# Kernel optimization log

Hardware: AMD Instinct MI355X
Metric: run time of the kernel (lower is better)

The kernel has to match this reference:

```python
import jax, jax.numpy as jnp
import numpy as np

B, S, D, H = 2, 2048, 1024, 16
DEPTH = D // H


def setup_inputs() -> dict:
    key = jax.random.key(0)
    ks = jax.random.split(key, 12)
    inp = {
        "q": jax.random.normal(ks[0], (B, S, D), jnp.float32),
        "k": jax.random.normal(ks[1], (B, S, D), jnp.float32),
        "v": jax.random.normal(ks[2], (B, S - 1, D), jnp.float32),
        # causal mask for the sliced (S-1, S-1) score grid: 1 where masked out
        "mask": jnp.broadcast_to(
            jnp.triu(jnp.ones((S - 1, S - 1), jnp.float32), k=1), (B, S - 1, S - 1)
        ),
        "Wq": jax.random.normal(ks[3], (D, D), jnp.float32) * 0.02,
        "bq": jnp.zeros((D,), jnp.float32),
        "Wk": jax.random.normal(ks[4], (D, D), jnp.float32) * 0.02,
        "bk": jnp.zeros((D,), jnp.float32),
        "Wv": jax.random.normal(ks[5], (D, D), jnp.float32) * 0.02,
        "bv": jnp.zeros((D,), jnp.float32),
        "Wo": jax.random.normal(ks[6], (D, D), jnp.float32) * 0.02,
        "bo": jnp.zeros((D,), jnp.float32),
    }
    return inp


def _split_heads(x):
    # (B, L, D) -> (B, H, L, depth)
    b, l, _ = x.shape
    return x.reshape(b, l, H, DEPTH).transpose(0, 2, 1, 3)


def reference(q, k, v, mask, Wq, bq, Wk, bk, Wv, bv, Wo, bo):
    qq = q @ Wq + bq            # q_layers[0]
    kk = k @ Wk + bk            # k_layers[0]
    vv = v @ Wv + bv            # wv
    qh, kh, vh = _split_heads(qq), _split_heads(kk), _split_heads(vv)
    # scores: (B, H, S, S) then sliced to (B, H, S-1, S-1) as in the source
    scores = jnp.einsum('bhqd,bhkd->bhqk', qh, kh)[:, :, 1:, :-1]
    scale = 1.0 / jnp.sqrt(jnp.asarray(DEPTH, jnp.float32))
    # original casts to fp64 here; JAX default x64-disabled => computed in fp32
    logits = scores * scale + mask[:, None, :, :] * (-1e9)
    att = jax.nn.softmax(logits, axis=-1)   # (B, H, S-1, S-1)
    ctx = jnp.einsum('bhqk,bhkd->bhqd', att, vh)  # v seq len is S-1
    ctx = ctx.transpose(0, 2, 1, 3).reshape(q.shape[0], -1, D)
    out = ctx @ Wo + bo
    return out, att
```

## Files before the change

### kernel.cpp

```cpp
#include <hip/hip_runtime.h>


typedef __attribute__((ext_vector_type(8))) short bf16x8;
typedef __attribute__((ext_vector_type(4))) float f32x4;

#define MFMA_BF16(A, B, C) __builtin_amdgcn_mfma_f32_16x16x32_bf16(A, B, C, 0, 0, 0)

__device__ __forceinline__ short f2bf(float x) {
    unsigned u = __float_as_uint(x);
    u = u + 0x7FFFu + ((u >> 16) & 1u);
    return (short)(u >> 16);
}
__device__ __forceinline__ float bf2f(short s) {
    return __uint_as_float(((unsigned)(unsigned short)s) << 16);
}
__device__ __forceinline__ int imin(int a, int b) { return a < b ? a : b; }

__global__ __launch_bounds__(256) void transpose_split_kernel(
    const float* __restrict__ W, short* __restrict__ Thi, short* __restrict__ Tlo) {
    __shared__ float tile[32][33];
    const int tx = threadIdx.x & 31, ty = threadIdx.x >> 5;
    const int k0 = blockIdx.x * 32, n0 = blockIdx.y * 32;
#pragma unroll
    for (int p = 0; p < 4; ++p)
        tile[ty + p * 8][tx] = W[(size_t)(k0 + ty + p * 8) * 1024 + n0 + tx];
    __syncthreads();
#pragma unroll
    for (int p = 0; p < 4; ++p) {
        int n = n0 + ty + p * 8, k = k0 + tx;
        float x = tile[tx][ty + p * 8];
        short h = f2bf(x);
        Thi[(size_t)n * 1024 + k] = h;
        if (Tlo) Tlo[(size_t)n * 1024 + k] = f2bf(x - bf2f(h));
    }
}

template <int SPLIT, int OUTMODE>
__global__ __launch_bounds__(256) void gemm_kernel(
    const float* __restrict__ A, int M,
    const short* __restrict__ Bthi, const short* __restrict__ Btlo,
    const float* __restrict__ bias,
    float* __restrict__ Cf, short* __restrict__ Chi, short* __restrict__ Clo) {
    __shared__ __align__(16) short Ash[64 * 40];
    __shared__ __align__(16) short Asl[64 * 40];
    __shared__ __align__(16) short Bsh[64 * 40];
    __shared__ __align__(16) short Bsl[64 * 40];

    const int tid = threadIdx.x;
    const int wave = tid >> 6, lane = tid & 63;
    const int quad = lane >> 4, l16 = lane & 15;
    const int m0 = blockIdx.y * 64, n0 = blockIdx.x * 64;

    const int row_s = tid >> 2;
    const int k_s = (tid & 3) * 8;

    f32x4 acc[4];
#pragma unroll
    for (int s = 0; s < 4; ++s) acc[s] = (f32x4){0.f, 0.f, 0.f, 0.f};

    for (int k0 = 0; k0 < 1024; k0 += 32) {
        __syncthreads();
        {
            int arow = imin(m0 + row_s, M - 1);
            const float* ap = A + (size_t)arow * 1024 + k0 + k_s;
            float4 x0 = *(const float4*)ap;
            float4 x1 = *(const float4*)(ap + 4);
            float xs[8] = {x0.x, x0.y, x0.z, x0.w, x1.x, x1.y, x1.z, x1.w};
            bf16x8 hv, lv;
#pragma unroll
            for (int i2 = 0; i2 < 8; ++i2) {
                short h = f2bf(xs[i2]);
                hv[i2] = h;
                if (SPLIT) lv[i2] = f2bf(xs[i2] - bf2f(h));
            }
            *(bf16x8*)&Ash[row_s * 40 + k_s] = hv;
            if (SPLIT) *(bf16x8*)&Asl[row_s * 40 + k_s] = lv;

            const short* bp = Bthi + (size_t)(n0 + row_s) * 1024 + k0 + k_s;
            *(bf16x8*)&Bsh[row_s * 40 + k_s] = *(const bf16x8*)bp;
            if (SPLIT) {
                const short* bp2 = Btlo + (size_t)(n0 + row_s) * 1024 + k0 + k_s;
                *(bf16x8*)&Bsl[row_s * 40 + k_s] = *(const bf16x8*)bp2;
            }
        }
        __syncthreads();

        bf16x8 ah = *(const bf16x8*)&Ash[(wave * 16 + l16) * 40 + quad * 8];
        bf16x8 al;
        if (SPLIT) al = *(const bf16x8*)&Asl[(wave * 16 + l16) * 40 + quad * 8];
#pragma unroll
        for (int s = 0; s < 4; ++s) {
            bf16x8 bh = *(const bf16x8*)&Bsh[(s * 16 + l16) * 40 + quad * 8];
            acc[s] = MFMA_BF16(ah, bh, acc[s]);
            if (SPLIT) {
                bf16x8 bl = *(const bf16x8*)&Bsl[(s * 16 + l16) * 40 + quad * 8];
                acc[s] = MFMA_BF16(ah, bl, acc[s]);
                acc[s] = MFMA_BF16(al, bh, acc[s]);
            }
        }
    }

#pragma unroll
    for (int s = 0; s < 4; ++s) {
        int col = n0 + s * 16 + l16;
        float bv = bias[col];
#pragma unroll
        for (int r = 0; r < 4; ++r) {
            int row = m0 + wave * 16 + quad * 4 + r;
            if (row < M) {
                float c = acc[s][r] + bv;
                size_t off = (size_t)row * 1024 + col;
                if (OUTMODE == 0) {
                    Cf[off] = c;
                } else if (OUTMODE == 1) {
                    Chi[off] = f2bf(c);
                } else {
                    short h = f2bf(c);
                    Chi[off] = h;
                    Clo[off] = f2bf(c - bf2f(h));
                }
            }
        }
    }
}

__global__ __launch_bounds__(256) void attn_kernel(
    const short* __restrict__ QQh, const short* __restrict__ QQl,
    const short* __restrict__ KKh, const short* __restrict__ KKl,
    const short* __restrict__ VV,
    float* __restrict__ att, float* __restrict__ ctx) {
    __shared__ __align__(16) short Ksh[32 * 72];
    __shared__ __align__(16) short Ksl[32 * 72];
    __shared__ __align__(16) short Vts[64 * 40];
    __shared__ __align__(16) short Ps[4][16 * 40];

    const int tid = threadIdx.x;
    const int wave = tid >> 6, lane = tid & 63;
    const int quad = lane >> 4, l16 = lane & 15;
    const int bx = blockIdx.x;
    const int qt = 31 - (bx & 31);
    const int bh = bx >> 5;
    const int h = bh & 15, b = bh >> 4;
    const int i0 = qt * 64;

    const int i_frag = i0 + wave * 16 + l16;
    const int qrow = imin(i_frag + 1, 2047);
    const size_t qoff = ((size_t)(b * 2048 + qrow)) * 1024 + h * 64;
    const bf16x8 qh0 = *(const bf16x8*)&QQh[qoff + 0 + quad * 8];
    const bf16x8 qh1 = *(const bf16x8*)&QQh[qoff + 32 + quad * 8];
    const bf16x8 ql0 = *(const bf16x8*)&QQl[qoff + 0 + quad * 8];
    const bf16x8 ql1 = *(const bf16x8*)&QQl[qoff + 32 + quad * 8];

    const int i_max = imin(i0 + 63, 2046);
    const int jt_max = i_max >> 5;
    const int wave_imax = imin(i0 + wave * 16 + 15, 2046);
    const int my_rowbase = i0 + wave * 16 + quad * 4;

    const int kst_key = tid >> 3;
    const int kst_dd = (tid & 7) * 8;
    const int vst_key = tid & 31, vst_d0 = (tid >> 5) * 8;

    float lsum[4] = {0.f, 0.f, 0.f, 0.f};

    for (int jt = 0; jt <= jt_max; ++jt) {
        __syncthreads();
        {
            int jg = imin(jt * 32 + kst_key, 2047);
            const size_t koff = ((size_t)(b * 2048 + jg)) * 1024 + h * 64 + kst_dd;
            *(bf16x8*)&Ksh[kst_key * 72 + kst_dd] = *(const bf16x8*)&KKh[koff];
            *(bf16x8*)&Ksl[kst_key * 72 + kst_dd] = *(const bf16x8*)&KKl[koff];
        }
        __syncthreads();
        if (jt * 32 <= wave_imax) {
#pragma unroll
            for (int s = 0; s < 2; ++s) {
                f32x4 sc = (f32x4){0.f, 0.f, 0.f, 0.f};
#pragma unroll
                for (int c = 0; c < 2; ++c) {
                    bf16x8 bh = *(const bf16x8*)&Ksh[(s * 16 + l16) * 72 + c * 32 + quad * 8];
                    bf16x8 bl = *(const bf16x8*)&Ksl[(s * 16 + l16) * 72 + c * 32 + quad * 8];
                    bf16x8 ah = (c == 0) ? qh0 : qh1;
                    bf16x8 al = (c == 0) ? ql0 : ql1;
                    sc = MFMA_BF16(ah, bh, sc);
                    sc = MFMA_BF16(ah, bl, sc);
                    sc = MFMA_BF16(al, bh, sc);
                }
                int j = jt * 32 + s * 16 + l16;
#pragma unroll
                for (int r = 0; r < 4; ++r) {
                    int i = my_rowbase + r;
                    if (j <= i && i <= 2046) lsum[r] += __expf(sc[r] * 0.125f);
                }
            }
        }
    }
#pragma unroll
    for (int m = 1; m < 16; m <<= 1) {
#pragma unroll
        for (int r = 0; r < 4; ++r) lsum[r] += __shfl_xor(lsum[r], m, 64);
    }
    float linv[4];
#pragma unroll
    for (int r = 0; r < 4; ++r) linv[r] = 1.0f / lsum[r];

    f32x4 cacc[4];
#pragma unroll
    for (int t = 0; t < 4; ++t) cacc[t] = (f32x4){0.f, 0.f, 0.f, 0.f};

    for (int jt = 0; jt <= jt_max; ++jt) {
        __syncthreads();
        {
            int jg = imin(jt * 32 + kst_key, 2047);
            const size_t koff = ((size_t)(b * 2048 + jg)) * 1024 + h * 64 + kst_dd;
            *(bf16x8*)&Ksh[kst_key * 72 + kst_dd] = *(const bf16x8*)&KKh[koff];
            *(bf16x8*)&Ksl[kst_key * 72 + kst_dd] = *(const bf16x8*)&KKl[koff];
            int vjg = imin(jt * 32 + vst_key, 2046);
            const size_t voff = ((size_t)(b * 2047 + vjg)) * 1024 + h * 64 + vst_d0;
            bf16x8 vv = *(const bf16x8*)&VV[voff];
#pragma unroll
            for (int q2 = 0; q2 < 8; ++q2) Vts[(vst_d0 + q2) * 40 + vst_key] = vv[q2];
        }
        __syncthreads();
        if (jt * 32 <= wave_imax) {
#pragma unroll
            for (int s = 0; s < 2; ++s) {
                f32x4 sc = (f32x4){0.f, 0.f, 0.f, 0.f};
#pragma unroll
                for (int c = 0; c < 2; ++c) {
                    bf16x8 bh = *(const bf16x8*)&Ksh[(s * 16 + l16) * 72 + c * 32 + quad * 8];
                    bf16x8 bl = *(const bf16x8*)&Ksl[(s * 16 + l16) * 72 + c * 32 + quad * 8];
                    bf16x8 ah = (c == 0) ? qh0 : qh1;
                    bf16x8 al = (c == 0) ? ql0 : ql1;
                    sc = MFMA_BF16(ah, bh, sc);
                    sc = MFMA_BF16(ah, bl, sc);
                    sc = MFMA_BF16(al, bh, sc);
                }
                int j = jt * 32 + s * 16 + l16;
#pragma unroll
                for (int r = 0; r < 4; ++r) {
                    int i = my_rowbase + r;
                    bool valid = (j <= i) && (i <= 2046);
                    float p = valid ? __expf(sc[r] * 0.125f) * linv[r] : 0.0f;
                    if (i <= 2046 && j <= 2046)
                        att[(((size_t)(b * 16 + h)) * 2047 + i) * 2047 + j] = p;
                    Ps[wave][(quad * 4 + r) * 40 + s * 16 + l16] = f2bf(p);
                }
            }
            bf16x8 pa = *(const bf16x8*)&Ps[wave][l16 * 40 + quad * 8];
#pragma unroll
            for (int t = 0; t < 4; ++t) {
                bf16x8 vb = *(const bf16x8*)&Vts[(t * 16 + l16) * 40 + quad * 8];
                cacc[t] = MFMA_BF16(pa, vb, cacc[t]);
            }
        } else {
#pragma unroll
            for (int s = 0; s < 2; ++s) {
                int j = jt * 32 + s * 16 + l16;
#pragma unroll
                for (int r = 0; r < 4; ++r) {
                    int i = my_rowbase + r;
                    if (i <= 2046 && j <= 2046)
                        att[(((size_t)(b * 16 + h)) * 2047 + i) * 2047 + j] = 0.0f;
                }
            }
        }
    }

#pragma unroll
    for (int t = 0; t < 4; ++t) {
#pragma unroll
        for (int r = 0; r < 4; ++r) {
            int i = my_rowbase + r;
            if (i <= 2046)
                ctx[((size_t)(b * 2047 + i)) * 1024 + h * 64 + t * 16 + l16] = cacc[t][r];
        }
    }

    const int js = (jt_max + 1) * 32;
    for (int rr = 0; rr < 64; ++rr) {
        int i = i0 + rr;
        if (i > 2046) break;
        float* rowp = att + (((size_t)(b * 16 + h)) * 2047 + i) * 2047;
        for (int cc = js + tid; cc < 2047; cc += 256) rowp[cc] = 0.0f;
    }
}

extern "C" void kernel_launch(void* const* d_in, const int* in_sizes, int n_in,
                              void* d_out, int out_size, void* d_ws, size_t ws_size,
                              hipStream_t stream) {
    (void)in_sizes; (void)n_in; (void)out_size; (void)ws_size;
    const float* q  = (const float*)d_in[0];
    const float* k  = (const float*)d_in[1];
    const float* v  = (const float*)d_in[2];
    const float* Wq = (const float*)d_in[4];
    const float* bq = (const float*)d_in[5];
    const float* Wk = (const float*)d_in[6];
    const float* bk = (const float*)d_in[7];
    const float* Wv = (const float*)d_in[8];
    const float* bv = (const float*)d_in[9];
    const float* Wo = (const float*)d_in[10];
    const float* bo = (const float*)d_in[11];

    float* out = (float*)d_out;
    float* att = out + (size_t)2 * 2047 * 1024;

    char* ws = (char*)d_ws;
    size_t off = 0;
    auto alloc = [&](size_t bytes) -> void* {
        void* p = ws + off;
        off += (bytes + 255) & ~(size_t)255;
        return p;
    };
    short* Wqt_h = (short*)alloc((size_t)1024 * 1024 * 2);
    short* Wqt_l = (short*)alloc((size_t)1024 * 1024 * 2);
    short* Wkt_h = (short*)alloc((size_t)1024 * 1024 * 2);
    short* Wkt_l = (short*)alloc((size_t)1024 * 1024 * 2);
    short* Wvt_h = (short*)alloc((size_t)1024 * 1024 * 2);
    short* Wot_h = (short*)alloc((size_t)1024 * 1024 * 2);
    short* QQh = (short*)alloc((size_t)4096 * 1024 * 2);
    short* QQl = (short*)alloc((size_t)4096 * 1024 * 2);
    short* KKh = (short*)alloc((size_t)4096 * 1024 * 2);
    short* KKl = (short*)alloc((size_t)4096 * 1024 * 2);
    short* VVp = (short*)alloc((size_t)4094 * 1024 * 2);
    float* CTX = (float*)alloc((size_t)4094 * 1024 * 4);

    dim3 tgrid(32, 32);
    transpose_split_kernel<<<tgrid, 256, 0, stream>>>(Wq, Wqt_h, Wqt_l);
    transpose_split_kernel<<<tgrid, 256, 0, stream>>>(Wk, Wkt_h, Wkt_l);
    transpose_split_kernel<<<tgrid, 256, 0, stream>>>(Wv, Wvt_h, nullptr);
    transpose_split_kernel<<<tgrid, 256, 0, stream>>>(Wo, Wot_h, nullptr);

    dim3 ggrid(16, 64);
    gemm_kernel<1, 2><<<ggrid, 256, 0, stream>>>(q, 4096, Wqt_h, Wqt_l, bq, nullptr, QQh, QQl);
    gemm_kernel<1, 2><<<ggrid, 256, 0, stream>>>(k, 4096, Wkt_h, Wkt_l, bk, nullptr, KKh, KKl);
    gemm_kernel<0, 1><<<ggrid, 256, 0, stream>>>(v, 4094, Wvt_h, nullptr, bv, nullptr, VVp, nullptr);

    attn_kernel<<<dim3(2 * 16 * 32), 256, 0, stream>>>(QQh, QQl, KKh, KKl, VVp, att, CTX);

    gemm_kernel<0, 0><<<ggrid, 256, 0, stream>>>(CTX, 4094, Wot_h, nullptr, bo, out, nullptr, nullptr);
}
```

Before: 1.049 ms.

## Rewrite pipeline with bf16 pre-split inputs, LDS DMA loads, larger tiles, transposed V

Inputs are split to bf16 hi/lo ahead of time so the GEMMs load pre-converted operands straight into LDS with global_load_lds DMA, using 128x64 tiles per block. The attention kernel moves to 64-key tiles and folds the 1/8 scale into the Q projection. Its first pass uses a 2-MFMA approximation for the row sums, V is pre-transposed so its tiles can also be DMA-loaded, and the context is written as bf16. These changes target conversion overhead, the LDS store cost and register shuffles, at the price of extra kernels and workspace. The cheaper row sums and bf16 context also reduce precision.

```diff
diff --git a/kernel.cpp b/kernel.cpp
--- a/kernel.cpp
+++ b/kernel.cpp
@@ -15,6 +15,12 @@
     return __uint_as_float(((unsigned)(unsigned short)s) << 16);
 }
 __device__ __forceinline__ int imin(int a, int b) { return a < b ? a : b; }
+
+__device__ __forceinline__ void dma16(const short* g, short* l) {
+    __builtin_amdgcn_global_load_lds(
+        (const __attribute__((address_space(1))) unsigned int*)g,
+        (__attribute__((address_space(3))) unsigned int*)l, 16, 0, 0);
+}
 
 __global__ __launch_bounds__(256) void transpose_split_kernel(
     const float* __restrict__ W, short* __restrict__ Thi, short* __restrict__ Tlo) {
@@ -35,115 +41,175 @@
     }
 }
 
+__global__ __launch_bounds__(256) void split_kernel(
+    const float* __restrict__ X, short* __restrict__ Hi, short* __restrict__ Lo, int n8) {
+    int idx = blockIdx.x * 256 + threadIdx.x;
+    if (idx >= n8) return;
+    float4 x0 = *((const float4*)X + (size_t)idx * 2);
+    float4 x1 = *((const float4*)X + (size_t)idx * 2 + 1);
+    float xs[8] = {x0.x, x0.y, x0.z, x0.w, x1.x, x1.y, x1.z, x1.w};
+    bf16x8 hv, lv;
+#pragma unroll
+    for (int e = 0; e < 8; ++e) {
+        short h = f2bf(xs[e]);
+        hv[e] = h;
+        lv[e] = f2bf(xs[e] - bf2f(h));
+    }
+    *(bf16x8*)&Hi[(size_t)idx * 8] = hv;
+    if (Lo) *(bf16x8*)&Lo[(size_t)idx * 8] = lv;
+}
+
 template <int SPLIT, int OUTMODE>
-__global__ __launch_bounds__(256) void gemm_kernel(
-    const float* __restrict__ A, int M,
-    const short* __restrict__ Bthi, const short* __restrict__ Btlo,
-    const float* __restrict__ bias,
+__global__ __launch_bounds__(256) void gemm_dma(
+    const short* __restrict__ Ahg, const short* __restrict__ Alg, int M,
+    const short* __restrict__ Bhg, const short* __restrict__ Blg,
+    const float* __restrict__ bias, float scale,
     float* __restrict__ Cf, short* __restrict__ Chi, short* __restrict__ Clo) {
-    __shared__ __align__(16) short Ash[64 * 40];
-    __shared__ __align__(16) short Asl[64 * 40];
-    __shared__ __align__(16) short Bsh[64 * 40];
-    __shared__ __align__(16) short Bsl[64 * 40];
+    __shared__ __align__(16) short Ah[512 * 8];
+    __shared__ __align__(16) short Al[SPLIT ? 512 * 8 : 8];
+    __shared__ __align__(16) short Bh[256 * 8];
+    __shared__ __align__(16) short Bl[SPLIT ? 256 * 8 : 8];
 
     const int tid = threadIdx.x;
-    const int wave = tid >> 6, lane = tid & 63;
+    const int w = tid >> 6, lane = tid & 63;
     const int quad = lane >> 4, l16 = lane & 15;
-    const int m0 = blockIdx.y * 64, n0 = blockIdx.x * 64;
-
-    const int row_s = tid >> 2;
-    const int k_s = (tid & 3) * 8;
-
-    f32x4 acc[4];
-#pragma unroll
-    for (int s = 0; s < 4; ++s) acc[s] = (f32x4){0.f, 0.f, 0.f, 0.f};
+    const int m0 = blockIdx.y * 128, n0 = blockIdx.x * 64;
+    const int row0 = (w & 1) * 64, col0 = (w >> 1) * 32;
+
+    f32x4 acc[4][2];
+#pragma unroll
+    for (int mi = 0; mi < 4; ++mi)
+#pragma unroll
+        for (int ni = 0; ni < 2; ++ni) acc[mi][ni] = (f32x4){0.f, 0.f, 0.f, 0.f};
+
+    const int a_row = tid & 127;
+    const int a_gr = imin(m0 + a_row, M - 1);
+    const int b_gr = n0 + (tid & 63);
+    const int b_c = tid >> 6;
 
     for (int k0 = 0; k0 < 1024; k0 += 32) {
         __syncthreads();
+#pragma unroll
+        for (int p = 0; p < 2; ++p) {
+            int c = (p * 256 + tid) >> 7;
+            const size_t go = (size_t)a_gr * 1024 + k0 + c * 8;
+            dma16(Ahg + go, &Ah[(p * 256 + tid) * 8]);
+            if (SPLIT) dma16(Alg + go, &Al[(p * 256 + tid) * 8]);
+        }
         {
-            int arow = imin(m0 + row_s, M - 1);
-            const float* ap = A + (size_t)arow * 1024 + k0 + k_s;
-            float4 x0 = *(const float4*)ap;
-            float4 x1 = *(const float4*)(ap + 4);
-            float xs[8] = {x0.x, x0.y, x0.z, x0.w, x1.x, x1.y, x1.z, x1.w};
-            bf16x8 hv, lv;
-#pragma unroll
-            for (int i2 = 0; i2 < 8; ++i2) {
-                short h = f2bf(xs[i2]);
-                hv[i2] = h;
-                if (SPLIT) lv[i2] = f2bf(xs[i2] - bf2f(h));
-            }
-            *(bf16x8*)&Ash[row_s * 40 + k_s] = hv;
-            if (SPLIT) *(bf16x8*)&Asl[row_s * 40 + k_s] = lv;
-
-            const short* bp = Bthi + (size_t)(n0 + row_s) * 1024 + k0 + k_s;
-            *(bf16x8*)&Bsh[row_s * 40 + k_s] = *(const bf16x8*)bp;
-            if (SPLIT) {
-                const short* bp2 = Btlo + (size_t)(n0 + row_s) * 1024 + k0 + k_s;
-                *(bf16x8*)&Bsl[row_s * 40 + k_s] = *(const bf16x8*)bp2;
-            }
-        }
-        __syncthreads();
-
-        bf16x8 ah = *(const bf16x8*)&Ash[(wave * 16 + l16) * 40 + quad * 8];
-        bf16x8 al;
-        if (SPLIT) al = *(const bf16x8*)&Asl[(wave * 16 + l16) * 40 + quad * 8];
-#pragma unroll
-        for (int s = 0; s < 4; ++s) {
-            bf16x8 bh = *(const bf16x8*)&Bsh[(s * 16 + l16) * 40 + quad * 8];
-            acc[s] = MFMA_BF16(ah, bh, acc[s]);
-            if (SPLIT) {
-                bf16x8 bl = *(const bf16x8*)&Bsl[(s * 16 + l16) * 40 + quad * 8];
-                acc[s] = MFMA_BF16(ah, bl, acc[s]);
-                acc[s] = MFMA_BF16(al, bh, acc[s]);
-            }
-        }
-    }
-
-#pragma unroll
-    for (int s = 0; s < 4; ++s) {
-        int col = n0 + s * 16 + l16;
+            const size_t go = (size_t)b_gr * 1024 + k0 + b_c * 8;
+            dma16(Bhg + go, &Bh[tid * 8]);
+            if (SPLIT) dma16(Blg + go, &Bl[tid * 8]);
+        }
+        __syncthreads();
+
+        bf16x8 af[4], afl[4], bfr[2], bfl[2];
+#pragma unroll
+        for (int mi = 0; mi < 4; ++mi) {
+            int r = row0 + mi * 16 + l16;
+            af[mi] = *(const bf16x8*)&Ah[(quad * 128 + r) * 8];
+            if (SPLIT) afl[mi] = *(const bf16x8*)&Al[(quad * 128 + r) * 8];
+        }
+#pragma unroll
+        for (int ni = 0; ni < 2; ++ni) {
+            int cdx = col0 + ni * 16 + l16;
+            bfr[ni] = *(const bf16x8*)&Bh[(quad * 64 + cdx) * 8];
+            if (SPLIT) bfl[ni] = *(const bf16x8*)&Bl[(quad * 64 + cdx) * 8];
+        }
+#pragma unroll
+        for (int mi = 0; mi < 4; ++mi)
+#pragma unroll
+            for (int ni = 0; ni < 2; ++ni) {
+                acc[mi][ni] = MFMA_BF16(af[mi], bfr[ni], acc[mi][ni]);
+                if (SPLIT) {
+                    acc[mi][ni] = MFMA_BF16(af[mi], bfl[ni], acc[mi][ni]);
+                    acc[mi][ni] = MFMA_BF16(afl[mi], bfr[ni], acc[mi][ni]);
+                }
+            }
+    }
+
+#pragma unroll
+    for (int ni = 0; ni < 2; ++ni) {
+        int col = n0 + col0 + ni * 16 + l16;
         float bv = bias[col];
 #pragma unroll
-        for (int r = 0; r < 4; ++r) {
-            int row = m0 + wave * 16 + quad * 4 + r;
-            if (row < M) {
-                float c = acc[s][r] + bv;
-                size_t off = (size_t)row * 1024 + col;
-                if (OUTMODE == 0) {
-                    Cf[off] = c;
-                } else if (OUTMODE == 1) {
-                    Chi[off] = f2bf(c);
-                } else {
-                    short h = f2bf(c);
-                    Chi[off] = h;
-                    Clo[off] = f2bf(c - bf2f(h));
-                }
-            }
-        }
+        for (int mi = 0; mi < 4; ++mi) {
+#pragma unroll
+            for (int r = 0; r < 4; ++r) {
+                int row = m0 + row0 + mi * 16 + quad * 4 + r;
+                if (row < M) {
+                    float c = (acc[mi][ni][r] + bv) * scale;
+                    size_t off = (size_t)row * 1024 + col;
+                    if (OUTMODE == 0) {
+                        Cf[off] = c;
+                    } else if (OUTMODE == 1) {
+                        Chi[off] = f2bf(c);
+                    } else {
+                        short h = f2bf(c);
+                        Chi[off] = h;
+                        Clo[off] = f2bf(c - bf2f(h));
+                    }
+                }
+            }
+        }
+    }
+}
+
+__global__ __launch_bounds__(256) void transpose_v_kernel(
+    const short* __restrict__ VV, short* __restrict__ VT) {
+    __shared__ short t[64][72];
+    const int tid = threadIdx.x;
+    const int st = blockIdx.x & 31, bh = blockIdx.x >> 5;
+    const int b = bh >> 4, h = bh & 15;
+    const int s0 = st * 64;
+    {
+        int seq = s0 + (tid >> 2), d0 = (tid & 3) * 16;
+        int seqc = imin(seq, 2046);
+        const short* src = VV + ((size_t)(b * 2047 + seqc)) * 1024 + h * 64 + d0;
+        bf16x8 v0 = *(const bf16x8*)src;
+        bf16x8 v1 = *(const bf16x8*)(src + 8);
+        bool ok = (seq <= 2046);
+#pragma unroll
+        for (int e = 0; e < 8; ++e) {
+            t[d0 + e][tid >> 2] = ok ? v0[e] : (short)0;
+            t[d0 + 8 + e][tid >> 2] = ok ? v1[e] : (short)0;
+        }
+    }
+    __syncthreads();
+    {
+        int d = tid >> 2, sc2 = (tid & 3) * 16;
+        bf16x8 o0, o1;
+#pragma unroll
+        for (int e = 0; e < 8; ++e) {
+            o0[e] = t[d][sc2 + e];
+            o1[e] = t[d][sc2 + 8 + e];
+        }
+        short* dst = VT + ((size_t)(bh * 64 + d)) * 2048 + s0 + sc2;
+        *(bf16x8*)dst = o0;
+        *(bf16x8*)(dst + 8) = o1;
     }
 }
 
 __global__ __launch_bounds__(256) void attn_kernel(
     const short* __restrict__ QQh, const short* __restrict__ QQl,
     const short* __restrict__ KKh, const short* __restrict__ KKl,
-    const short* __restrict__ VV,
-    float* __restrict__ att, float* __restrict__ ctx) {
-    __shared__ __align__(16) short Ksh[32 * 72];
-    __shared__ __align__(16) short Ksl[32 * 72];
-    __shared__ __align__(16) short Vts[64 * 40];
-    __shared__ __align__(16) short Ps[4][16 * 40];
+    const short* __restrict__ VT,
+    float* __restrict__ att, short* __restrict__ CTX) {
+    __shared__ __align__(16) short Kh[512 * 8];
+    __shared__ __align__(16) short Kl[512 * 8];
+    __shared__ __align__(16) short Vt[512 * 8];
+    __shared__ __align__(16) short Ps[4][16 * 72];
 
     const int tid = threadIdx.x;
-    const int wave = tid >> 6, lane = tid & 63;
+    const int w = tid >> 6, lane = tid & 63;
     const int quad = lane >> 4, l16 = lane & 15;
     const int bx = blockIdx.x;
-    const int qt = 31 - (bx & 31);
-    const int bh = bx >> 5;
+    const int qt = 31 - (bx >> 5);
+    const int bh = bx & 31;
     const int h = bh & 15, b = bh >> 4;
     const int i0 = qt * 64;
 
-    const int i_frag = i0 + wave * 16 + l16;
+    const int i_frag = i0 + w * 16 + l16;
     const int qrow = imin(i_frag + 1, 2047);
     const size_t qoff = ((size_t)(b * 2048 + qrow)) * 1024 + h * 64;
     const bf16x8 qh0 = *(const bf16x8*)&QQh[qoff + 0 + quad * 8];
@@ -152,44 +218,40 @@
     const bf16x8 ql1 = *(const bf16x8*)&QQl[qoff + 32 + quad * 8];
 
     const int i_max = imin(i0 + 63, 2046);
-    const int jt_max = i_max >> 5;
-    const int wave_imax = imin(i0 + wave * 16 + 15, 2046);
-    const int my_rowbase = i0 + wave * 16 + quad * 4;
-
-    const int kst_key = tid >> 3;
-    const int kst_dd = (tid & 7) * 8;
-    const int vst_key = tid & 31, vst_d0 = (tid >> 5) * 8;
+    const int jt_max = i_max >> 6;
+    const int wave_imax = imin(i0 + w * 16 + 15, 2046);
+    const int rowbase = i0 + w * 16 + quad * 4;
+
+    const int dma_key = tid & 63;
+    const int dma_cc0 = tid >> 6;
 
     float lsum[4] = {0.f, 0.f, 0.f, 0.f};
 
     for (int jt = 0; jt <= jt_max; ++jt) {
-        __syncthreads();
-        {
-            int jg = imin(jt * 32 + kst_key, 2047);
-            const size_t koff = ((size_t)(b * 2048 + jg)) * 1024 + h * 64 + kst_dd;
-            *(bf16x8*)&Ksh[kst_key * 72 + kst_dd] = *(const bf16x8*)&KKh[koff];
-            *(bf16x8*)&Ksl[kst_key * 72 + kst_dd] = *(const bf16x8*)&KKl[koff];
-        }
-        __syncthreads();
-        if (jt * 32 <= wave_imax) {
-#pragma unroll
-            for (int s = 0; s < 2; ++s) {
+        const int j0 = jt * 64;
+        __syncthreads();
+#pragma unroll
+        for (int p = 0; p < 2; ++p) {
+            int cc = p * 4 + dma_cc0;
+            dma16(KKh + ((size_t)(b * 2048 + j0 + dma_key)) * 1024 + h * 64 + cc * 8,
+                  &Kh[(p * 256 + tid) * 8]);
+        }
+        __syncthreads();
+        if (j0 <= wave_imax) {
+#pragma unroll
+            for (int s = 0; s < 4; ++s) {
                 f32x4 sc = (f32x4){0.f, 0.f, 0.f, 0.f};
 #pragma unroll
                 for (int c = 0; c < 2; ++c) {
-                    bf16x8 bh = *(const bf16x8*)&Ksh[(s * 16 + l16) * 72 + c * 32 + quad * 8];
-                    bf16x8 bl = *(const bf16x8*)&Ksl[(s * 16 + l16) * 72 + c * 32 + quad * 8];
-                    bf16x8 ah = (c == 0) ? qh0 : qh1;
-                    bf16x8 al = (c == 0) ? ql0 : ql1;
-                    sc = MFMA_BF16(ah, bh, sc);
-                    sc = MFMA_BF16(ah, bl, sc);
-                    sc = MFMA_BF16(al, bh, sc);
-                }
-                int j = jt * 32 + s * 16 + l16;
+                    bf16x8 kh = *(const bf16x8*)&Kh[((c * 4 + quad) * 64 + s * 16 + l16) * 8];
+                    sc = MFMA_BF16(c ? qh1 : qh0, kh, sc);
+                    sc = MFMA_BF16(c ? ql1 : ql0, kh, sc);
+                }
+                int j = j0 + s * 16 + l16;
 #pragma unroll
                 for (int r = 0; r < 4; ++r) {
-                    int i = my_rowbase + r;
-                    if (j <= i && i <= 2046) lsum[r] += __expf(sc[r] * 0.125f);
+                    int i = rowbase + r;
+                    if (j <= i && i <= 2046) lsum[r] += __expf(sc[r]);
                 }
             }
         }
@@ -208,59 +270,62 @@
     for (int t = 0; t < 4; ++t) cacc[t] = (f32x4){0.f, 0.f, 0.f, 0.f};
 
     for (int jt = 0; jt <= jt_max; ++jt) {
-        __syncthreads();
-        {
-            int jg = imin(jt * 32 + kst_key, 2047);
-            const size_t koff = ((size_t)(b * 2048 + jg)) * 1024 + h * 64 + kst_dd;
-            *(bf16x8*)&Ksh[kst_key * 72 + kst_dd] = *(const bf16x8*)&KKh[koff];
-            *(bf16x8*)&Ksl[kst_key * 72 + kst_dd] = *(const bf16x8*)&KKl[koff];
-            int vjg = imin(jt * 32 + vst_key, 2046);
-            const size_t voff = ((size_t)(b * 2047 + vjg)) * 1024 + h * 64 + vst_d0;
-            bf16x8 vv = *(const bf16x8*)&VV[voff];
-#pragma unroll
-            for (int q2 = 0; q2 < 8; ++q2) Vts[(vst_d0 + q2) * 40 + vst_key] = vv[q2];
-        }
-        __syncthreads();
-        if (jt * 32 <= wave_imax) {
-#pragma unroll
-            for (int s = 0; s < 2; ++s) {
+        const int j0 = jt * 64;
+        __syncthreads();
+#pragma unroll
+        for (int p = 0; p < 2; ++p) {
+            int cc = p * 4 + dma_cc0;
+            const size_t ko = ((size_t)(b * 2048 + j0 + dma_key)) * 1024 + h * 64 + cc * 8;
+            dma16(KKh + ko, &Kh[(p * 256 + tid) * 8]);
+            dma16(KKl + ko, &Kl[(p * 256 + tid) * 8]);
+            dma16(VT + ((size_t)(bh * 64 + dma_key)) * 2048 + j0 + cc * 8,
+                  &Vt[(p * 256 + tid) * 8]);
+        }
+        __syncthreads();
+        if (j0 <= wave_imax) {
+#pragma unroll
+            for (int s = 0; s < 4; ++s) {
                 f32x4 sc = (f32x4){0.f, 0.f, 0.f, 0.f};
 #pragma unroll
                 for (int c = 0; c < 2; ++c) {
-                    bf16x8 bh = *(const bf16x8*)&Ksh[(s * 16 + l16) * 72 + c * 32 + quad * 8];
-                    bf16x8 bl = *(const bf16x8*)&Ksl[(s * 16 + l16) * 72 + c * 32 + quad * 8];
-                    bf16x8 ah = (c == 0) ? qh0 : qh1;
-                    bf16x8 al = (c == 0) ? ql0 : ql1;
-                    sc = MFMA_BF16(ah, bh, sc);
-                    sc = MFMA_BF16(ah, bl, sc);
-                    sc = MFMA_BF16(al, bh, sc);
-                }
-                int j = jt * 32 + s * 16 + l16;
+                    const int ci = ((c * 4 + quad) * 64 + s * 16 + l16) * 8;
+                    bf16x8 kh = *(const bf16x8*)&Kh[ci];
+                    bf16x8 kl = *(const bf16x8*)&Kl[ci];
+                    bf16x8 ah = c ? qh1 : qh0;
+                    bf16x8 al = c ? ql1 : ql0;
+                    sc = MFMA_BF16(ah, kh, sc);
+                    sc = MFMA_BF16(ah, kl, sc);
+                    sc = MFMA_BF16(al, kh, sc);
+                }
+                int j = j0 + s * 16 + l16;
 #pragma unroll
                 for (int r = 0; r < 4; ++r) {
-                    int i = my_rowbase + r;
+                    int i = rowbase + r;
                     bool valid = (j <= i) && (i <= 2046);
-                    float p = valid ? __expf(sc[r] * 0.125f) * linv[r] : 0.0f;
+                    float p = valid ? __expf(sc[r]) * linv[r] : 0.0f;
                     if (i <= 2046 && j <= 2046)
-                        att[(((size_t)(b * 16 + h)) * 2047 + i) * 2047 + j] = p;
-                    Ps[wave][(quad * 4 + r) * 40 + s * 16 + l16] = f2bf(p);
-                }
-            }
-            bf16x8 pa = *(const bf16x8*)&Ps[wave][l16 * 40 + quad * 8];
-#pragma unroll
-            for (int t = 0; t < 4; ++t) {
-                bf16x8 vb = *(const bf16x8*)&Vts[(t * 16 + l16) * 40 + quad * 8];
-                cacc[t] = MFMA_BF16(pa, vb, cacc[t]);
+                        att[((size_t)bh * 2047 + i) * 2047 + j] = p;
+                    Ps[w][(quad * 4 + r) * 72 + s * 16 + l16] = f2bf(p);
+                }
+            }
+#pragma unroll
+            for (int c = 0; c < 2; ++c) {
+                bf16x8 pa = *(const bf16x8*)&Ps[w][l16 * 72 + c * 32 + quad * 8];
+#pragma unroll
+                for (int t = 0; t < 4; ++t) {
+                    bf16x8 vb = *(const bf16x8*)&Vt[((c * 4 + quad) * 64 + t * 16 + l16) * 8];
+                    cacc[t] = MFMA_BF16(pa, vb, cacc[t]);
+                }
             }
         } else {
 #pragma unroll
-            for (int s = 0; s < 2; ++s) {
-                int j = jt * 32 + s * 16 + l16;
+            for (int s = 0; s < 4; ++s) {
+                int j = j0 + s * 16 + l16;
 #pragma unroll
                 for (int r = 0; r < 4; ++r) {
-                    int i = my_rowbase + r;
+                    int i = rowbase + r;
                     if (i <= 2046 && j <= 2046)
-                        att[(((size_t)(b * 16 + h)) * 2047 + i) * 2047 + j] = 0.0f;
+                        att[((size_t)bh * 2047 + i) * 2047 + j] = 0.0f;
                 }
             }
         }
@@ -270,18 +335,16 @@
     for (int t = 0; t < 4; ++t) {
 #pragma unroll
         for (int r = 0; r < 4; ++r) {
-            int i = my_rowbase + r;
+            int i = rowbase + r;
             if (i <= 2046)
-                ctx[((size_t)(b * 2047 + i)) * 1024 + h * 64 + t * 16 + l16] = cacc[t][r];
-        }
-    }
-
-    const int js = (jt_max + 1) * 32;
-    for (int rr = 0; rr < 64; ++rr) {
-        int i = i0 + rr;
-        if (i > 2046) break;
-        float* rowp = att + (((size_t)(b * 16 + h)) * 2047 + i) * 2047;
-        for (int cc = js + tid; cc < 2047; cc += 256) rowp[cc] = 0.0f;
+                CTX[((size_t)(b * 2047 + i)) * 1024 + h * 64 + t * 16 + l16] = f2bf(cacc[t][r]);
+        }
+    }
+
+    const int js = (jt_max + 1) * 64;
+    for (int i = i0; i <= i_max; ++i) {
+        float* rowp = att + ((size_t)bh * 2047 + i) * 2047;
+        for (int cc2 = js + tid; cc2 < 2047; cc2 += 256) rowp[cc2] = 0.0f;
     }
 }
 
@@ -317,12 +380,18 @@
     short* Wkt_l = (short*)alloc((size_t)1024 * 1024 * 2);
     short* Wvt_h = (short*)alloc((size_t)1024 * 1024 * 2);
     short* Wot_h = (short*)alloc((size_t)1024 * 1024 * 2);
+    short* Qhi = (short*)alloc((size_t)4096 * 1024 * 2);
+    short* Qlo = (short*)alloc((size_t)4096 * 1024 * 2);
+    short* Khi = (short*)alloc((size_t)4096 * 1024 * 2);
+    short* Klo = (short*)alloc((size_t)4096 * 1024 * 2);
+    short* Vbf = (short*)alloc((size_t)4096 * 1024 * 2);
     short* QQh = (short*)alloc((size_t)4096 * 1024 * 2);
     short* QQl = (short*)alloc((size_t)4096 * 1024 * 2);
     short* KKh = (short*)alloc((size_t)4096 * 1024 * 2);
     short* KKl = (short*)alloc((size_t)4096 * 1024 * 2);
-    short* VVp = (short*)alloc((size_t)4094 * 1024 * 2);
-    float* CTX = (float*)alloc((size_t)4094 * 1024 * 4);
+    short* VV  = (short*)alloc((size_t)4096 * 1024 * 2);
+    short* VT  = (short*)alloc((size_t)2048 * 2048 * 2 * 2);
+    short* CTX = (short*)alloc((size_t)4096 * 1024 * 2);
 
     dim3 tgrid(32, 32);
     transpose_split_kernel<<<tgrid, 256, 0, stream>>>(Wq, Wqt_h, Wqt_l);
@@ -330,12 +399,22 @@
     transpose_split_kernel<<<tgrid, 256, 0, stream>>>(Wv, Wvt_h, nullptr);
     transpose_split_kernel<<<tgrid, 256, 0, stream>>>(Wo, Wot_h, nullptr);
 
-    dim3 ggrid(16, 64);
-    gemm_kernel<1, 2><<<ggrid, 256, 0, stream>>>(q, 4096, Wqt_h, Wqt_l, bq, nullptr, QQh, QQl);
-    gemm_kernel<1, 2><<<ggrid, 256, 0, stream>>>(k, 4096, Wkt_h, Wkt_l, bk, nullptr, KKh, KKl);
-    gemm_kernel<0, 1><<<ggrid, 256, 0, stream>>>(v, 4094, Wvt_h, nullptr, bv, nullptr, VVp, nullptr);
-
-    attn_kernel<<<dim3(2 * 16 * 32), 256, 0, stream>>>(QQh, QQl, KKh, KKl, VVp, att, CTX);
-
-    gemm_kernel<0, 0><<<ggrid, 256, 0, stream>>>(CTX, 4094, Wot_h, nullptr, bo, out, nullptr, nullptr);
-}
+    split_kernel<<<2048, 256, 0, stream>>>(q, Qhi, Qlo, 4096 * 1024 / 8);
+    split_kernel<<<2048, 256, 0, stream>>>(k, Khi, Klo, 4096 * 1024 / 8);
+    split_kernel<<<2047, 256, 0, stream>>>(v, Vbf, nullptr, 4094 * 1024 / 8);
+
+    dim3 ggrid(16, 32);
+    gemm_dma<1, 2><<<ggrid, 256, 0, stream>>>(Qhi, Qlo, 4096, Wqt_h, Wqt_l, bq, 0.125f,
+                                              nullptr, QQh, QQl);
+    gemm_dma<1, 2><<<ggrid, 256, 0, stream>>>(Khi, Klo, 4096, Wkt_h, Wkt_l, bk, 1.0f,
+                                              nullptr, KKh, KKl);
+    gemm_dma<0, 1><<<ggrid, 256, 0, stream>>>(Vbf, nullptr, 4094, Wvt_h, nullptr, bv, 1.0f,
+                                              nullptr, VV, nullptr);
+
+    transpose_v_kernel<<<dim3(32 * 32), 256, 0, stream>>>(VV, VT);
+
+    attn_kernel<<<dim3(32 * 32), 256, 0, stream>>>(QQh, QQl, KKh, KKl, VT, att, CTX);
+
+    gemm_dma<0, 0><<<ggrid, 256, 0, stream>>>(CTX, nullptr, 4094, Wot_h, nullptr, bo, 1.0f,
+                                              out, nullptr, nullptr);
+}
```

Result: faster. 995.3 us (-5.1%).
